# Optimization experiments

Measured on AMD Instinct MI355X. Metric: run time of the kernel, lower is better.

The kernel has to match this reference:

```python
import jax, jax.numpy as jnp
import numpy as np

H = 8
D = 64
EPS = 1e-5
TEMP = 1.0


def _ln(x, w, b):
    m = jnp.mean(x, axis=-1, keepdims=True)
    v = jnp.var(x, axis=-1, keepdims=True)
    return (x - m) * jax.lax.rsqrt(v + EPS) * w + b


def setup_inputs() -> dict:
    key = jax.random.key(0)
    ks = jax.random.split(key, 8)
    B, T, C = 4, 1024, 512
    x = jax.random.normal(ks[0], (B, T, C), dtype=jnp.float32)
    pair = jax.random.normal(ks[1], (B, T, T, H), dtype=jnp.float32)
    mask = jax.random.randint(ks[2], (B, T, T), 0, 2).astype(bool)
    s = 0.02
    return {
        "x": x,
        "pair": pair,
        "mask": mask,
        "norm_w": jnp.ones((C,), jnp.float32),
        "norm_b": jnp.zeros((C,), jnp.float32),
        "qkv_w": jax.random.normal(ks[3], (3 * C, C), jnp.float32) * s,
        "qkv_b": jnp.zeros((3 * C,), jnp.float32),
        "qln_w": jnp.ones((C,), jnp.float32),
        "qln_b": jnp.zeros((C,), jnp.float32),
        "kln_w": jnp.ones((C,), jnp.float32),
        "kln_b": jnp.zeros((C,), jnp.float32),
        "proj_w": jax.random.normal(ks[4], (C, C), jnp.float32) * s,
        "proj_b": jnp.zeros((C,), jnp.float32),
    }


def reference(x, pair, mask, norm_w, norm_b, qkv_w, qkv_b, qln_w, qln_b,
              kln_w, kln_b, proj_w, proj_b):
    B, T, C = x.shape
    # pre-norm
    xn = _ln(x, norm_w, norm_b)
    qkv = xn @ qkv_w.T + qkv_b  # [B,T,3C]
    q, k, v = jnp.split(qkv, 3, axis=-1)
    q = _ln(q, qln_w, qln_b)
    k = _ln(k, kln_w, kln_b)
    # [B,T,C] -> [B,H,T,D]
    to_heads = lambda t: t.reshape(B, T, H, D).transpose(0, 2, 1, 3)
    q, k, v = to_heads(q), to_heads(k), to_heads(v)
    scale = (D ** -0.5) / TEMP
    sim = jnp.einsum("bhid,bhjd->bhij", q, k) * scale
    sim = sim + pair.transpose(0, 3, 1, 2)  # additive pair bias [B,H,T,T]
    neg = jnp.finfo(sim.dtype).min
    sim = jnp.where(mask[:, None, :, :], sim, sim + neg)
    attn = jax.nn.softmax(sim, axis=-1)
    out = jnp.einsum("bhij,bhjd->bhid", attn, v)
    out = out.transpose(0, 2, 1, 3).reshape(B, T, C)
    return out @ proj_w.T + proj_b
```

## Files before the change

kernel.cpp:

```cpp
#include <hip/hip_runtime.h>
#include <math.h>

#define B_  4
#define T_  1024
#define C_  512
#define H_  8
#define D_  64
#define N3_ 1536
#define BT_ 4096

constexpr float kEps = 1e-5f;
constexpr float kNeg = -3.4028234663852886e38f;
constexpr float kMaskNeg = -1.4e38f;
constexpr float kLog2e = 1.44269504088896f;
constexpr float kShift2 = 17.312340490667562f;

typedef __attribute__((ext_vector_type(8))) short bf16x8;
typedef __attribute__((ext_vector_type(4))) float f32x4;

__device__ __forceinline__ short f2bf(float f) {
  union { float f; unsigned u; } v; v.f = f;
  unsigned r = v.u + 0x7FFFu + ((v.u >> 16) & 1u);
  return (short)(r >> 16);
}
__device__ __forceinline__ float bf2f(unsigned short b) {
  union { unsigned u; float f; } v;
  v.u = ((unsigned)b) << 16;
  return v.f;
}

__device__ __forceinline__ void gld16(const void* g, void* l) {
  __builtin_amdgcn_global_load_lds(
      (const __attribute__((address_space(1))) unsigned int*)g,
      (__attribute__((address_space(3))) unsigned int*)l, 16, 0, 0);
}

__global__ __launch_bounds__(64) void mask_detect_kernel(
    const unsigned int* __restrict__ m, int* __restrict__ flag) {
  int lane = threadIdx.x;
  int any_big = 0;
#pragma unroll
  for (int p = 0; p < 16; ++p) {
    unsigned int v = m[lane + p * 64];
    any_big |= (v > 1u);
  }
  unsigned long long b = __ballot(any_big);
  if (lane == 0) flag[0] = (b != 0ull) ? 1 : 0;
}

__global__ __launch_bounds__(256) void mask_convert_kernel(
    const void* __restrict__ mraw, const int* __restrict__ flag,
    uchar4* __restrict__ out) {
  int idx = blockIdx.x * 256 + threadIdx.x;
  uchar4 v;
  if (flag[0]) {
    v = ((const uchar4*)mraw)[idx];
    v.x = v.x ? 1 : 0; v.y = v.y ? 1 : 0; v.z = v.z ? 1 : 0; v.w = v.w ? 1 : 0;
  } else {
    int4 w = ((const int4*)mraw)[idx];
    v = make_uchar4(w.x != 0, w.y != 0, w.z != 0, w.w != 0);
  }
  out[idx] = v;
}

__global__ __launch_bounds__(256) void pair_prep_kernel(
    const float* __restrict__ pair, const void* __restrict__ mraw,
    short* __restrict__ biast) {
  __shared__ short P[8][1024 + 8];
  unsigned wv = ((const unsigned*)mraw)[threadIdx.x];
  int is_u8 = __syncthreads_or(wv > 1u);
  int bi = blockIdx.x;
  int b = bi >> 10, i = bi & 1023;
  int tid = threadIdx.x;
  const float* src = pair + (size_t)bi * (T_ * H_);
#pragma unroll
  for (int p = 0; p < 8; ++p) {
    int c = tid + p * 256;
    int j = c >> 1, hh = (c & 1) * 4;
    float4 v = *(const float4*)&src[c * 4];
    P[hh + 0][j] = f2bf(v.x * kLog2e);
    P[hh + 1][j] = f2bf(v.y * kLog2e);
    P[hh + 2][j] = f2bf(v.z * kLog2e);
    P[hh + 3][j] = f2bf(v.w * kLog2e);
  }
  bool mk[4];
  if (is_u8) {
    uchar4 mv = ((const uchar4*)mraw)[bi * 256 + tid];
    mk[0] = mv.x; mk[1] = mv.y; mk[2] = mv.z; mk[3] = mv.w;
  } else {
    int4 mv = ((const int4*)mraw)[bi * 256 + tid];
    mk[0] = mv.x != 0; mk[1] = mv.y != 0; mk[2] = mv.z != 0; mk[3] = mv.w != 0;
  }
  __syncthreads();
  const short negb = f2bf(kMaskNeg);
  int j = tid * 4;
#pragma unroll
  for (int h = 0; h < 8; ++h) {
    short4 o;
    o.x = mk[0] ? P[h][j + 0] : negb;
    o.y = mk[1] ? P[h][j + 1] : negb;
    o.z = mk[2] ? P[h][j + 2] : negb;
    o.w = mk[3] ? P[h][j + 3] : negb;
    *(short4*)&biast[((size_t)(b * 8 + h) * T_ + i) * T_ + j] = o;
  }
}

__global__ __launch_bounds__(256) void wcvt2_kernel(
    const float* __restrict__ a, short* __restrict__ oa,
    const float* __restrict__ b, short* __restrict__ ob, int nblk_a) {
  int bid = blockIdx.x;
  const float* src; short* dst; int idx;
  if (bid < nblk_a) { src = a; dst = oa; idx = bid * 256 + threadIdx.x; }
  else             { src = b; dst = ob; idx = (bid - nblk_a) * 256 + threadIdx.x; }
  int i = idx * 4;
  float4 v = *(const float4*)&src[i];
  short4 o;
  o.x = f2bf(v.x); o.y = f2bf(v.y); o.z = f2bf(v.z); o.w = f2bf(v.w);
  *(short4*)&dst[i] = o;
}

__global__ __launch_bounds__(128) void ln_x_kernel(
    const float* __restrict__ x, const float* __restrict__ w,
    const float* __restrict__ b, short* __restrict__ xn) {
  int row = blockIdx.x;
  int tid = threadIdx.x;
  const float* xr = x + (size_t)row * C_;
  float4 v = *(const float4*)&xr[tid * 4];
  float s  = v.x + v.y + v.z + v.w;
  float ss = v.x * v.x + v.y * v.y + v.z * v.z + v.w * v.w;
#pragma unroll
  for (int o = 32; o > 0; o >>= 1) {
    s  += __shfl_down(s, o);
    ss += __shfl_down(ss, o);
  }
  __shared__ float sh[4];
  int wid = tid >> 6, lane = tid & 63;
  if (lane == 0) { sh[wid] = s; sh[2 + wid] = ss; }
  __syncthreads();
  float m   = (sh[0] + sh[1]) * (1.0f / C_);
  float var = (sh[2] + sh[3]) * (1.0f / C_) - m * m;
  float inv = rsqrtf(var + kEps);
  float4 wv = *(const float4*)&w[tid * 4];
  float4 bv = *(const float4*)&b[tid * 4];
  short4 o4;
  o4.x = f2bf((v.x - m) * inv * wv.x + bv.x);
  o4.y = f2bf((v.y - m) * inv * wv.y + bv.y);
  o4.z = f2bf((v.z - m) * inv * wv.z + bv.z);
  o4.w = f2bf((v.w - m) * inv * wv.w + bv.w);
  *(short4*)&xn[(size_t)row * C_ + tid * 4] = o4;
}

__global__ __launch_bounds__(256) void gemm_bf16_kernel(
    const short* __restrict__ A, const short* __restrict__ W,
    const float* __restrict__ bias, float* __restrict__ Cmat,
    int M, int N, int K) {
  __shared__ short As[128 * 64];
  __shared__ short Bs[64 * 64];
  int tid = threadIdx.x;
  int lane = tid & 63, wave = tid >> 6;
  int wm = wave >> 1, wn = wave & 1;
  int col = lane & 15, quad = lane >> 4;
  int m0 = blockIdx.y * 128, n0 = blockIdx.x * 64;
  int wbase = tid & ~63;

  f32x4 acc[4][2];
#pragma unroll
  for (int mi = 0; mi < 4; ++mi)
#pragma unroll
    for (int ni = 0; ni < 2; ++ni) acc[mi][ni] = {0.f, 0.f, 0.f, 0.f};

  for (int k0 = 0; k0 < K; k0 += 64) {
    __syncthreads();
#pragma unroll
    for (int p = 0; p < 4; ++p) {
      int c = tid + p * 256;
      int row = c >> 3, kc = (c & 7) * 8;
      gld16(&A[(size_t)(m0 + row) * K + k0 + kc], &As[(wbase + p * 256) * 8]);
    }
#pragma unroll
    for (int p = 0; p < 2; ++p) {
      int c = tid + p * 256;
      int row = c >> 3, kc = (c & 7) * 8;
      gld16(&W[(size_t)(n0 + row) * K + k0 + kc], &Bs[(wbase + p * 256) * 8]);
    }
    __syncthreads();
#pragma unroll
    for (int s = 0; s < 2; ++s) {
      bf16x8 af[4], bfv[2];
#pragma unroll
      for (int mi = 0; mi < 4; ++mi)
        af[mi] = *(const bf16x8*)&As[(64 * wm + 16 * mi + col) * 64 + s * 32 + quad * 8];
#pragma unroll
      for (int ni = 0; ni < 2; ++ni)
        bfv[ni] = *(const bf16x8*)&Bs[(32 * wn + 16 * ni + col) * 64 + s * 32 + quad * 8];
#pragma unroll
      for (int mi = 0; mi < 4; ++mi)
#pragma unroll
        for (int ni = 0; ni < 2; ++ni)
          acc[mi][ni] = __builtin_amdgcn_mfma_f32_16x16x32_bf16(
              af[mi], bfv[ni], acc[mi][ni], 0, 0, 0);
    }
  }
#pragma unroll
  for (int ni = 0; ni < 2; ++ni) {
    int n = n0 + 32 * wn + 16 * ni + col;
    float bv = bias[n];
#pragma unroll
    for (int mi = 0; mi < 4; ++mi) {
#pragma unroll
      for (int r = 0; r < 4; ++r) {
        int m = m0 + 64 * wm + 16 * mi + quad * 4 + r;
        Cmat[(size_t)m * N + n] = acc[mi][ni][r] + bv;
      }
    }
  }
}

__global__ __launch_bounds__(128) void qkv_ln_split_kernel(
    const float* __restrict__ qkv,
    const float* __restrict__ qw, const float* __restrict__ qb,
    const float* __restrict__ kw, const float* __restrict__ kb,
    short* __restrict__ qh, short* __restrict__ kh, short* __restrict__ vh) {
  int row = blockIdx.x;
  int b = row >> 10, t = row & 1023;
  int tid = threadIdx.x;
  const float* base = qkv + (size_t)row * N3_;
  int c4 = tid * 4;
  float4 qv = *(const float4*)&base[c4];
  float4 kv = *(const float4*)&base[C_ + c4];
  float4 vv = *(const float4*)&base[2 * C_ + c4];
  float sq  = qv.x + qv.y + qv.z + qv.w;
  float sqq = qv.x * qv.x + qv.y * qv.y + qv.z * qv.z + qv.w * qv.w;
  float sk  = kv.x + kv.y + kv.z + kv.w;
  float skk = kv.x * kv.x + kv.y * kv.y + kv.z * kv.z + kv.w * kv.w;
#pragma unroll
  for (int o = 32; o > 0; o >>= 1) {
    sq  += __shfl_down(sq, o);
    sqq += __shfl_down(sqq, o);
    sk  += __shfl_down(sk, o);
    skk += __shfl_down(skk, o);
  }
  __shared__ float sh[8];
  int wid = tid >> 6, lane = tid & 63;
  if (lane == 0) { sh[wid] = sq; sh[2 + wid] = sqq; sh[4 + wid] = sk; sh[6 + wid] = skk; }
  __syncthreads();
  float qm   = (sh[0] + sh[1]) * (1.0f / C_);
  float qvar = (sh[2] + sh[3]) * (1.0f / C_) - qm * qm;
  float km   = (sh[4] + sh[5]) * (1.0f / C_);
  float kvar = (sh[6] + sh[7]) * (1.0f / C_) - km * km;
  float qi = rsqrtf(qvar + kEps);
  float ki = rsqrtf(kvar + kEps);
  float4 qwv = *(const float4*)&qw[c4];
  float4 qbv = *(const float4*)&qb[c4];
  float4 kwv = *(const float4*)&kw[c4];
  float4 kbv = *(const float4*)&kb[c4];
  int h = tid >> 4;
  int d = (tid & 15) * 4;
  size_t dst = ((size_t)(b * H_ + h) * T_ + t) * D_ + d;
  short4 qo, ko, vo;
  qo.x = f2bf(((qv.x - qm) * qi * qwv.x + qbv.x) * 0.125f);
  qo.y = f2bf(((qv.y - qm) * qi * qwv.y + qbv.y) * 0.125f);
  qo.z = f2bf(((qv.z - qm) * qi * qwv.z + qbv.z) * 0.125f);
  qo.w = f2bf(((qv.w - qm) * qi * qwv.w + qbv.w) * 0.125f);
  ko.x = f2bf((kv.x - km) * ki * kwv.x + kbv.x);
  ko.y = f2bf((kv.y - km) * ki * kwv.y + kbv.y);
  ko.z = f2bf((kv.z - km) * ki * kwv.z + kbv.z);
  ko.w = f2bf((kv.w - km) * ki * kwv.w + kbv.w);
  vo.x = f2bf(vv.x); vo.y = f2bf(vv.y); vo.z = f2bf(vv.z); vo.w = f2bf(vv.w);
  *(short4*)&qh[dst] = qo;
  *(short4*)&kh[dst] = ko;
  *(short4*)&vh[dst] = vo;
}

__global__ __launch_bounds__(256) void attn_split_kernel(
    const short* __restrict__ qh, const short* __restrict__ kh,
    const short* __restrict__ vh, const short* __restrict__ biast,
    float* __restrict__ Opart, float* __restrict__ lpart) {
  __shared__ short Ks[64 * 72];
  __shared__ short Vt[64 * 72];
  __shared__ short Ps[64 * 72];
  int tid = threadIdx.x;
  int lane = tid & 63, w = tid >> 6;
  int col = lane & 15, quad = lane >> 4;
  int bh = blockIdx.y;
  int half = blockIdx.z;
  int i0 = blockIdx.x * 64;
  const short* Qg = qh + (size_t)bh * T_ * D_;
  const short* Kg = kh + (size_t)bh * T_ * D_;
  const short* Vg = vh + (size_t)bh * T_ * D_;
  const unsigned short* Bpu =
      (const unsigned short*)(biast + (size_t)bh * T_ * T_);

  bf16x8 qf[2];
#pragma unroll
  for (int s = 0; s < 2; ++s)
    qf[s] = *(const bf16x8*)&Qg[(size_t)(i0 + 16 * w + col) * D_ + s * 32 + quad * 8];

  float lsum[4];
  f32x4 oacc[4];
#pragma unroll
  for (int r = 0; r < 4; ++r) lsum[r] = 0.f;
#pragma unroll
  for (int dt = 0; dt < 4; ++dt) oacc[dt] = {0.f, 0.f, 0.f, 0.f};

  int jbase = half * (T_ / 2);
  for (int jj = 0; jj < T_ / 2; jj += 64) {
    int j0 = jbase + jj;
    __syncthreads();
#pragma unroll
    for (int p = 0; p < 2; ++p) {
      int c = tid + p * 256;
      int row = c >> 3, dc = (c & 7) * 8;
      *(int4*)&Ks[row * 72 + dc] =
          *(const int4*)&Kg[(size_t)(j0 + row) * D_ + dc];
    }
    {
      int j = tid & 63, d0 = (tid >> 6) * 16;
#pragma unroll
      for (int p = 0; p < 2; ++p) {
        short tmp[8];
        *(int4*)tmp = *(const int4*)&Vg[(size_t)(j0 + j) * D_ + d0 + p * 8];
#pragma unroll
        for (int q = 0; q < 8; ++q) Vt[(d0 + p * 8 + q) * 72 + j] = tmp[q];
      }
    }
    __syncthreads();

    unsigned short bsv[4][4];
#pragma unroll
    for (int r = 0; r < 4; ++r) {
      int gi = i0 + 16 * w + quad * 4 + r;
#pragma unroll
      for (int jt = 0; jt < 4; ++jt)
        bsv[r][jt] = Bpu[(size_t)gi * T_ + j0 + 16 * jt + col];
    }

    f32x4 sacc[4];
#pragma unroll
    for (int jt = 0; jt < 4; ++jt) sacc[jt] = {0.f, 0.f, 0.f, 0.f};
#pragma unroll
    for (int s = 0; s < 2; ++s) {
#pragma unroll
      for (int jt = 0; jt < 4; ++jt) {
        bf16x8 kf = *(const bf16x8*)&Ks[(16 * jt + col) * 72 + s * 32 + quad * 8];
        sacc[jt] = __builtin_amdgcn_mfma_f32_16x16x32_bf16(qf[s], kf, sacc[jt], 0, 0, 0);
      }
    }

#pragma unroll
    for (int r = 0; r < 4; ++r) {
      int li = 16 * w + quad * 4 + r;
#pragma unroll
      for (int jt = 0; jt < 4; ++jt) {
        float sv = fmaf(sacc[jt][r], kLog2e, bf2f(bsv[r][jt]));
        float p = exp2f(fminf(sv - kShift2, 86.5f));
        lsum[r] += p;
        Ps[li * 72 + 16 * jt + col] = f2bf(p);
      }
    }

#pragma unroll
    for (int s = 0; s < 2; ++s) {
      bf16x8 pf = *(const bf16x8*)&Ps[(16 * w + col) * 72 + s * 32 + quad * 8];
#pragma unroll
      for (int dt = 0; dt < 4; ++dt) {
        bf16x8 vf = *(const bf16x8*)&Vt[(16 * dt + col) * 72 + s * 32 + quad * 8];
        oacc[dt] = __builtin_amdgcn_mfma_f32_16x16x32_bf16(pf, vf, oacc[dt], 0, 0, 0);
      }
    }
  }

#pragma unroll
  for (int r = 0; r < 4; ++r) {
    float l = lsum[r];
#pragma unroll
    for (int o = 1; o < 16; o <<= 1) l += __shfl_xor(l, o);
    int gi = i0 + 16 * w + quad * 4 + r;
    size_t orow = (size_t)half * 32768 + (size_t)bh * T_ + gi;
    if (col == 0) lpart[orow] = l;
#pragma unroll
    for (int dt = 0; dt < 4; ++dt)
      Opart[orow * 64 + 16 * dt + col] = oacc[dt][r];
  }
}

__global__ __launch_bounds__(256) void attn_merge_kernel(
    const float* __restrict__ Opart, const float* __restrict__ lpart,
    short* __restrict__ ao) {
  int g = blockIdx.x * 256 + threadIdx.x;
  int row = g >> 4, d4 = (g & 15) * 4;
  float4 o0 = *(const float4*)&Opart[(size_t)row * 64 + d4];
  float4 o1 = *(const float4*)&Opart[((size_t)32768 + row) * 64 + d4];
  float inv = 1.0f / (lpart[row] + lpart[32768 + row]);
  int bh = row >> 10, gi = row & 1023;
  int b = bh >> 3, h = bh & 7;
  short4 o;
  o.x = f2bf((o0.x + o1.x) * inv);
  o.y = f2bf((o0.y + o1.y) * inv);
  o.z = f2bf((o0.z + o1.z) * inv);
  o.w = f2bf((o0.w + o1.w) * inv);
  *(short4*)&ao[((size_t)(b * T_ + gi)) * C_ + h * D_ + d4] = o;
}

__global__ __launch_bounds__(256) void attn_kernel(
    const short* __restrict__ qh, const short* __restrict__ kh,
    const short* __restrict__ vh, const float* __restrict__ pair,
    const unsigned char* __restrict__ mask, short* __restrict__ ao) {
  __shared__ short Ks[64 * 72];
  __shared__ short Vt[64 * 72];
  __shared__ short Ps[64 * 72];
  int tid = threadIdx.x;
  int lane = tid & 63, w = tid >> 6;
  int col = lane & 15, quad = lane >> 4;
  int bh = blockIdx.y;
  int b = bh >> 3, h = bh & 7;
  int i0 = blockIdx.x * 64;
  const short* Qg = qh + (size_t)bh * T_ * D_;
  const short* Kg = kh + (size_t)bh * T_ * D_;
  const short* Vg = vh + (size_t)bh * T_ * D_;

  bf16x8 qf[2];
#pragma unroll
  for (int s = 0; s < 2; ++s)
    qf[s] = *(const bf16x8*)&Qg[(size_t)(i0 + 16 * w + col) * D_ + s * 32 + quad * 8];

  float mrun[4], lrun[4];
  f32x4 oacc[4];
#pragma unroll
  for (int r = 0; r < 4; ++r) { mrun[r] = -INFINITY; lrun[r] = 0.f; }
#pragma unroll
  for (int dt = 0; dt < 4; ++dt) oacc[dt] = {0.f, 0.f, 0.f, 0.f};

  for (int j0 = 0; j0 < T_; j0 += 64) {
    __syncthreads();
#pragma unroll
    for (int p = 0; p < 2; ++p) {
      int c = tid + p * 256;
      int row = c >> 3, dc = (c & 7) * 8;
      *(int4*)&Ks[row * 72 + dc] =
          *(const int4*)&Kg[(size_t)(j0 + row) * D_ + dc];
    }
    {
      int j = tid & 63, d0 = (tid >> 6) * 16;
#pragma unroll
      for (int p = 0; p < 2; ++p) {
        short tmp[8];
        *(int4*)tmp = *(const int4*)&Vg[(size_t)(j0 + j) * D_ + d0 + p * 8];
#pragma unroll
        for (int q = 0; q < 8; ++q) Vt[(d0 + p * 8 + q) * 72 + j] = tmp[q];
      }
    }
    __syncthreads();

    f32x4 sacc[4];
#pragma unroll
    for (int jt = 0; jt < 4; ++jt) sacc[jt] = {0.f, 0.f, 0.f, 0.f};
#pragma unroll
    for (int s = 0; s < 2; ++s) {
#pragma unroll
      for (int jt = 0; jt < 4; ++jt) {
        bf16x8 kf = *(const bf16x8*)&Ks[(16 * jt + col) * 72 + s * 32 + quad * 8];
        sacc[jt] = __builtin_amdgcn_mfma_f32_16x16x32_bf16(qf[s], kf, sacc[jt], 0, 0, 0);
      }
    }

#pragma unroll
    for (int r = 0; r < 4; ++r) {
      int gi = i0 + 16 * w + quad * 4 + r;
      const float* prow = pair + (size_t)(b * T_ + gi) * (T_ * H_) + h;
      const unsigned char* mrow = mask + (size_t)(b * T_ + gi) * T_;
      float sv[4];
      float rm = -INFINITY;
#pragma unroll
      for (int jt = 0; jt < 4; ++jt) {
        int j = j0 + 16 * jt + col;
        float s = sacc[jt][r] + prow[(size_t)j * H_];
        if (!mrow[j]) s += kNeg;
        sv[jt] = s;
        rm = fmaxf(rm, s);
      }
#pragma unroll
      for (int o = 8; o > 0; o >>= 1) rm = fmaxf(rm, __shfl_xor(rm, o));
      float mnew  = fmaxf(mrun[r], rm);
      float alpha = __expf(mrun[r] - mnew);
      float psum = 0.f;
#pragma unroll
      for (int jt = 0; jt < 4; ++jt) {
        float p = __expf(sv[jt] - mnew);
        psum += p;
        Ps[(16 * w + quad * 4 + r) * 72 + 16 * jt + col] = f2bf(p);
      }
#pragma unroll
      for (int o = 8; o > 0; o >>= 1) psum += __shfl_xor(psum, o);
      lrun[r] = lrun[r] * alpha + psum;
      mrun[r] = mnew;
#pragma unroll
      for (int dt = 0; dt < 4; ++dt) oacc[dt][r] *= alpha;
    }
    __syncthreads();

#pragma unroll
    for (int s = 0; s < 2; ++s) {
      bf16x8 pf = *(const bf16x8*)&Ps[(16 * w + col) * 72 + s * 32 + quad * 8];
#pragma unroll
      for (int dt = 0; dt < 4; ++dt) {
        bf16x8 vf = *(const bf16x8*)&Vt[(16 * dt + col) * 72 + s * 32 + quad * 8];
        oacc[dt] = __builtin_amdgcn_mfma_f32_16x16x32_bf16(pf, vf, oacc[dt], 0, 0, 0);
      }
    }
  }

#pragma unroll
  for (int r = 0; r < 4; ++r) {
    int gi = i0 + 16 * w + quad * 4 + r;
    float inv = 1.0f / lrun[r];
    size_t base = (size_t)(b * T_ + gi) * C_ + h * D_;
#pragma unroll
    for (int dt = 0; dt < 4; ++dt)
      ao[base + 16 * dt + col] = f2bf(oacc[dt][r] * inv);
  }
}

extern "C" void kernel_launch(void* const* d_in, const int* in_sizes, int n_in,
                              void* d_out, int out_size, void* d_ws, size_t ws_size,
                              hipStream_t stream) {
  const float* x      = (const float*)d_in[0];
  const float* pair   = (const float*)d_in[1];
  const void*  maskraw = d_in[2];
  const float* norm_w = (const float*)d_in[3];
  const float* norm_b = (const float*)d_in[4];
  const float* qkv_w  = (const float*)d_in[5];
  const float* qkv_b  = (const float*)d_in[6];
  const float* qln_w  = (const float*)d_in[7];
  const float* qln_b  = (const float*)d_in[8];
  const float* kln_w  = (const float*)d_in[9];
  const float* kln_b  = (const float*)d_in[10];
  const float* proj_w = (const float*)d_in[11];
  const float* proj_b = (const float*)d_in[12];
  float* out = (float*)d_out;

  short* xn = (short*)d_out;
  short* qh = (short*)d_out + (size_t)BT_ * C_;

  const size_t MB = 1024 * 1024;

  if (ws_size >= 96 * MB) {
    char* base = (char*)d_ws;
    short* biast = (short*)base;
    float* qkv   = (float*)base;
    float* Opart = (float*)(base + 64 * MB);
    float* lpart = (float*)(base + 80 * MB);
    short* ao    = (short*)(base + 81 * MB);
    short* kh    = (short*)(base + 85 * MB);
    short* vh    = (short*)(base + 89 * MB);
    short* wq    = (short*)(base + 93 * MB);
    short* wp    = (short*)(base + 94 * MB + 512 * 1024);

    wcvt2_kernel<<<(N3_ * C_ + C_ * C_) / 1024, 256, 0, stream>>>(
        qkv_w, wq, proj_w, wp, (N3_ * C_) / 1024);
    ln_x_kernel<<<BT_, 128, 0, stream>>>(x, norm_w, norm_b, xn);
    gemm_bf16_kernel<<<dim3(N3_ / 64, BT_ / 128), 256, 0, stream>>>(
        xn, wq, qkv_b, qkv, BT_, N3_, C_);
    qkv_ln_split_kernel<<<BT_, 128, 0, stream>>>(
        qkv, qln_w, qln_b, kln_w, kln_b, qh, kh, vh);
    pair_prep_kernel<<<B_ * T_, 256, 0, stream>>>(pair, maskraw, biast);
    attn_split_kernel<<<dim3(T_ / 64, B_ * H_, 2), 256, 0, stream>>>(
        qh, kh, vh, biast, Opart, lpart);
    attn_merge_kernel<<<2048, 256, 0, stream>>>(Opart, lpart, ao);
    gemm_bf16_kernel<<<dim3(C_ / 64, BT_ / 128), 256, 0, stream>>>(
        ao, wp, proj_b, out, BT_, C_, C_);
  } else {
    float* qkv = (float*)d_ws;
    short* ao  = (short*)d_ws;
    short* sw  = (short*)d_ws;
    short* wq  = sw + (size_t)12 * 1024 * 1024;
    short* wp  = wq + (size_t)N3_ * C_;
    short* kh  = sw + (size_t)13 * 1024 * 1024;
    short* vh  = sw + (size_t)15 * 1024 * 1024;
    unsigned char* maskc = (unsigned char*)d_ws + (size_t)34 * MB;
    int* flag = (int*)((unsigned char*)d_ws + (size_t)38 * MB);

    mask_detect_kernel<<<1, 64, 0, stream>>>((const unsigned int*)maskraw, flag);
    mask_convert_kernel<<<(B_ * T_ * T_) / 1024, 256, 0, stream>>>(
        maskraw, flag, (uchar4*)maskc);
    wcvt2_kernel<<<(N3_ * C_ + C_ * C_) / 1024, 256, 0, stream>>>(
        qkv_w, wq, proj_w, wp, (N3_ * C_) / 1024);
    ln_x_kernel<<<BT_, 128, 0, stream>>>(x, norm_w, norm_b, xn);
    gemm_bf16_kernel<<<dim3(N3_ / 64, BT_ / 128), 256, 0, stream>>>(
        xn, wq, qkv_b, qkv, BT_, N3_, C_);
    qkv_ln_split_kernel<<<BT_, 128, 0, stream>>>(
        qkv, qln_w, qln_b, kln_w, kln_b, qh, kh, vh);
    attn_kernel<<<dim3(T_ / 64, B_ * H_), 256, 0, stream>>>(
        qh, kh, vh, pair, maskc, ao);
    gemm_bf16_kernel<<<dim3(C_ / 64, BT_ / 128), 256, 0, stream>>>(
        ao, wp, proj_b, out, BT_, C_, C_);
  }
}
```

Before: 313.3 us.

## Fuse LN with weight conversion and fold attention merge into projection GEMM

Combines the input LayerNorm and the weight-to-bf16 conversion into a single launch. It also removes the separate attention split-merge kernel: the output projection GEMM now reads both fp32 partial outputs and the row sums directly, normalizes them and converts to bf16 while filling its A tile. This drops two launches and the write and re-read of the bf16 attention output. In exchange, each of the 8 column blocks re-reads the fp32 partials and recomputes the merge, and the A-tile load is now synchronous global reads instead of the async gld16 path.

```diff
diff --git a/kernel.cpp b/kernel.cpp
--- a/kernel.cpp
+++ b/kernel.cpp
@@ -150,6 +150,51 @@
   *(short4*)&xn[(size_t)row * C_ + tid * 4] = o4;
 }
 
+__global__ __launch_bounds__(128) void prep_fused_kernel(
+    const float* __restrict__ x, const float* __restrict__ nw,
+    const float* __restrict__ nb, short* __restrict__ xn,
+    const float* __restrict__ qkv_w, short* __restrict__ wq,
+    const float* __restrict__ proj_w, short* __restrict__ wp) {
+  int bid = blockIdx.x;
+  int tid = threadIdx.x;
+  if (bid < BT_) {
+    const float* xr = x + (size_t)bid * C_;
+    float4 v = *(const float4*)&xr[tid * 4];
+    float s  = v.x + v.y + v.z + v.w;
+    float ss = v.x * v.x + v.y * v.y + v.z * v.z + v.w * v.w;
+#pragma unroll
+    for (int o = 32; o > 0; o >>= 1) {
+      s  += __shfl_down(s, o);
+      ss += __shfl_down(ss, o);
+    }
+    __shared__ float sh[4];
+    int wid = tid >> 6, lane = tid & 63;
+    if (lane == 0) { sh[wid] = s; sh[2 + wid] = ss; }
+    __syncthreads();
+    float m   = (sh[0] + sh[1]) * (1.0f / C_);
+    float var = (sh[2] + sh[3]) * (1.0f / C_) - m * m;
+    float inv = rsqrtf(var + kEps);
+    float4 wv = *(const float4*)&nw[tid * 4];
+    float4 bv = *(const float4*)&nb[tid * 4];
+    short4 o4;
+    o4.x = f2bf((v.x - m) * inv * wv.x + bv.x);
+    o4.y = f2bf((v.y - m) * inv * wv.y + bv.y);
+    o4.z = f2bf((v.z - m) * inv * wv.z + bv.z);
+    o4.w = f2bf((v.w - m) * inv * wv.w + bv.w);
+    *(short4*)&xn[(size_t)bid * C_ + tid * 4] = o4;
+  } else {
+    int idx = (bid - BT_) * 128 + tid;
+    const float* src; short* dst;
+    if (idx < (N3_ * C_) / 4) { src = qkv_w; dst = wq; }
+    else { src = proj_w; dst = wp; idx -= (N3_ * C_) / 4; }
+    int i = idx * 4;
+    float4 v = *(const float4*)&src[i];
+    short4 o;
+    o.x = f2bf(v.x); o.y = f2bf(v.y); o.z = f2bf(v.z); o.w = f2bf(v.w);
+    *(short4*)&dst[i] = o;
+  }
+}
+
 __global__ __launch_bounds__(256) void gemm_bf16_kernel(
     const short* __restrict__ A, const short* __restrict__ W,
     const float* __restrict__ bias, float* __restrict__ Cmat,
@@ -211,6 +256,90 @@
       for (int r = 0; r < 4; ++r) {
         int m = m0 + 64 * wm + 16 * mi + quad * 4 + r;
         Cmat[(size_t)m * N + n] = acc[mi][ni][r] + bv;
+      }
+    }
+  }
+}
+
+__global__ __launch_bounds__(256) void gemm2_merge_kernel(
+    const float* __restrict__ Opart, const float* __restrict__ lpart,
+    const short* __restrict__ W, const float* __restrict__ bias,
+    float* __restrict__ Cmat) {
+  __shared__ short As[128 * 64];
+  __shared__ short Bs[64 * 64];
+  int tid = threadIdx.x;
+  int lane = tid & 63, wave = tid >> 6;
+  int wm = wave >> 1, wn = wave & 1;
+  int col = lane & 15, quad = lane >> 4;
+  int m0 = blockIdx.y * 128, n0 = blockIdx.x * 64;
+  int wbase = tid & ~63;
+
+  f32x4 acc[4][2];
+#pragma unroll
+  for (int mi = 0; mi < 4; ++mi)
+#pragma unroll
+    for (int ni = 0; ni < 2; ++ni) acc[mi][ni] = {0.f, 0.f, 0.f, 0.f};
+
+  for (int kt = 0; kt < 8; ++kt) {
+    __syncthreads();
+#pragma unroll
+    for (int p = 0; p < 4; ++p) {
+      int c = tid + p * 256;
+      int row = c >> 3, dc = (c & 7) * 8;
+      int m = m0 + row;
+      size_t orow = (size_t)((m >> 10) * 8 + kt) * 1024 + (m & 1023);
+      const float* s0 = &Opart[orow * 64 + dc];
+      const float* s1 = &Opart[((size_t)32768 + orow) * 64 + dc];
+      float inv = 1.0f / (lpart[orow] + lpart[32768 + orow]);
+      float4 a0 = *(const float4*)s0;
+      float4 a1 = *(const float4*)(s0 + 4);
+      float4 b0 = *(const float4*)s1;
+      float4 b1 = *(const float4*)(s1 + 4);
+      short o8[8];
+      o8[0] = f2bf((a0.x + b0.x) * inv);
+      o8[1] = f2bf((a0.y + b0.y) * inv);
+      o8[2] = f2bf((a0.z + b0.z) * inv);
+      o8[3] = f2bf((a0.w + b0.w) * inv);
+      o8[4] = f2bf((a1.x + b1.x) * inv);
+      o8[5] = f2bf((a1.y + b1.y) * inv);
+      o8[6] = f2bf((a1.z + b1.z) * inv);
+      o8[7] = f2bf((a1.w + b1.w) * inv);
+      *(int4*)&As[row * 64 + dc] = *(const int4*)o8;
+    }
+#pragma unroll
+    for (int p = 0; p < 2; ++p) {
+      int c = tid + p * 256;
+      int row = c >> 3, kc = (c & 7) * 8;
+      gld16(&W[(size_t)(n0 + row) * C_ + kt * 64 + kc], &Bs[(wbase + p * 256) * 8]);
+    }
+    __syncthreads();
+#pragma unroll
+    for (int s = 0; s < 2; ++s) {
+      bf16x8 af[4], bfv[2];
+#pragma unroll
+      for (int mi = 0; mi < 4; ++mi)
+        af[mi] = *(const bf16x8*)&As[(64 * wm + 16 * mi + col) * 64 + s * 32 + quad * 8];
+#pragma unroll
+      for (int ni = 0; ni < 2; ++ni)
+        bfv[ni] = *(const bf16x8*)&Bs[(32 * wn + 16 * ni + col) * 64 + s * 32 + quad * 8];
+#pragma unroll
+      for (int mi = 0; mi < 4; ++mi)
+#pragma unroll
+        for (int ni = 0; ni < 2; ++ni)
+          acc[mi][ni] = __builtin_amdgcn_mfma_f32_16x16x32_bf16(
+              af[mi], bfv[ni], acc[mi][ni], 0, 0, 0);
+    }
+  }
+#pragma unroll
+  for (int ni = 0; ni < 2; ++ni) {
+    int n = n0 + 32 * wn + 16 * ni + col;
+    float bv = bias[n];
+#pragma unroll
+    for (int mi = 0; mi < 4; ++mi) {
+#pragma unroll
+      for (int r = 0; r < 4; ++r) {
+        int m = m0 + 64 * wm + 16 * mi + quad * 4 + r;
+        Cmat[(size_t)m * C_ + n] = acc[mi][ni][r] + bv;
       }
     }
   }
@@ -384,24 +513,6 @@
   }
 }
 
-__global__ __launch_bounds__(256) void attn_merge_kernel(
-    const float* __restrict__ Opart, const float* __restrict__ lpart,
-    short* __restrict__ ao) {
-  int g = blockIdx.x * 256 + threadIdx.x;
-  int row = g >> 4, d4 = (g & 15) * 4;
-  float4 o0 = *(const float4*)&Opart[(size_t)row * 64 + d4];
-  float4 o1 = *(const float4*)&Opart[((size_t)32768 + row) * 64 + d4];
-  float inv = 1.0f / (lpart[row] + lpart[32768 + row]);
-  int bh = row >> 10, gi = row & 1023;
-  int b = bh >> 3, h = bh & 7;
-  short4 o;
-  o.x = f2bf((o0.x + o1.x) * inv);
-  o.y = f2bf((o0.y + o1.y) * inv);
-  o.z = f2bf((o0.z + o1.z) * inv);
-  o.w = f2bf((o0.w + o1.w) * inv);
-  *(short4*)&ao[((size_t)(b * T_ + gi)) * C_ + h * D_ + d4] = o;
-}
-
 __global__ __launch_bounds__(256) void attn_kernel(
     const short* __restrict__ qh, const short* __restrict__ kh,
     const short* __restrict__ vh, const float* __restrict__ pair,
@@ -550,15 +661,13 @@
     float* qkv   = (float*)base;
     float* Opart = (float*)(base + 64 * MB);
     float* lpart = (float*)(base + 80 * MB);
-    short* ao    = (short*)(base + 81 * MB);
     short* kh    = (short*)(base + 85 * MB);
     short* vh    = (short*)(base + 89 * MB);
     short* wq    = (short*)(base + 93 * MB);
     short* wp    = (short*)(base + 94 * MB + 512 * 1024);
 
-    wcvt2_kernel<<<(N3_ * C_ + C_ * C_) / 1024, 256, 0, stream>>>(
-        qkv_w, wq, proj_w, wp, (N3_ * C_) / 1024);
-    ln_x_kernel<<<BT_, 128, 0, stream>>>(x, norm_w, norm_b, xn);
+    prep_fused_kernel<<<BT_ + (N3_ * C_ + C_ * C_) / 512, 128, 0, stream>>>(
+        x, norm_w, norm_b, xn, qkv_w, wq, proj_w, wp);
     gemm_bf16_kernel<<<dim3(N3_ / 64, BT_ / 128), 256, 0, stream>>>(
         xn, wq, qkv_b, qkv, BT_, N3_, C_);
     qkv_ln_split_kernel<<<BT_, 128, 0, stream>>>(
@@ -566,9 +675,8 @@
     pair_prep_kernel<<<B_ * T_, 256, 0, stream>>>(pair, maskraw, biast);
     attn_split_kernel<<<dim3(T_ / 64, B_ * H_, 2), 256, 0, stream>>>(
         qh, kh, vh, biast, Opart, lpart);
-    attn_merge_kernel<<<2048, 256, 0, stream>>>(Opart, lpart, ao);
-    gemm_bf16_kernel<<<dim3(C_ / 64, BT_ / 128), 256, 0, stream>>>(
-        ao, wp, proj_b, out, BT_, C_, C_);
+    gemm2_merge_kernel<<<dim3(C_ / 64, BT_ / 128), 256, 0, stream>>>(
+        Opart, lpart, wp, proj_b, out);
   } else {
     float* qkv = (float*)d_ws;
     short* ao  = (short*)d_ws;
```

Result: slower. 329.9 us (+5.3%).
